# Optimization experiments

Measured on AMD Instinct MI355X. Metric: run time of the kernel, lower is better.

The kernel has to match this reference:

```python
import jax, jax.numpy as jnp
from jax import lax
import numpy as np

T_NO = 50       # history / kernel half-length (hard-coded in module)
T_MAX = 101     # basis kernel length = 2*T_NO + 1
BASIS_NO = 34
HIST_BASIS_NO = 18
SIGMA = 3.0
HID = 20
SUB = 20


def _make_basis(n_basis, length):
    # basis[i, t] = exp(-(t - 3*i)^2 / sigma)
    raw = jnp.arange(length, dtype=jnp.float32)
    pts = 3.0 * jnp.arange(n_basis, dtype=jnp.float32)
    return jnp.exp(-((raw[None, :] - pts[:, None]) ** 2) / SIGMA)


def _conv1d(x, kern, pad):
    # x: [1, Cin, T], kern: [Cout, Cin, K] -> [1, Cout, T'] (torch F.conv1d semantics, cross-correlation)
    return lax.conv_general_dilated(x, kern, window_strides=(1,), padding=[(pad, pad)],
                                    dimension_numbers=('NCH', 'OIH', 'NCH'))


def setup_inputs() -> dict:
    key = jax.random.key(0)
    ks = jax.random.split(key, 12)
    T, Ee, Ei = 200000, 500, 100
    S_e = (jax.random.uniform(ks[0], (T, Ee)) < 0.05).astype(jnp.float32)
    S_i = (jax.random.uniform(ks[1], (T, Ei)) < 0.05).astype(jnp.float32)
    # one-hot synapse->subunit connectivity, as in the original model
    C_syn_e = jax.nn.one_hot(jax.random.randint(ks[2], (Ee,), 0, SUB), SUB, dtype=jnp.float32).T
    C_syn_i = jax.nn.one_hot(jax.random.randint(ks[3], (Ei,), 0, SUB), SUB, dtype=jnp.float32).T
    weight1 = 0.01 * jax.random.normal(ks[4], (HID, 2 * SUB, BASIS_NO), dtype=jnp.float32)
    weight4 = 0.01 * jax.random.normal(ks[5], (1, HID, BASIS_NO), dtype=jnp.float32)
    W_hist = 0.01 * jax.random.normal(ks[6], (HIST_BASIS_NO,), dtype=jnp.float32)
    Theta = 0.01 * jax.random.normal(ks[7], (1,), dtype=jnp.float32)
    W_spk = jnp.ones((1,), jnp.float32)
    Tau_spk = 3.0 * jnp.ones((1,), jnp.float32)
    u = jax.random.uniform(ks[8], (T,), dtype=jnp.float32)  # bernoulli noise
    return dict(S_e=S_e, S_i=S_i, C_syn_e=C_syn_e, C_syn_i=C_syn_i,
                weight1=weight1, weight4=weight4, W_hist=W_hist, Theta=Theta,
                W_spk=W_spk, Tau_spk=Tau_spk, u=u)


def reference(S_e, S_i, C_syn_e, C_syn_i, weight1, weight4, W_hist, Theta, W_spk, Tau_spk, u):
    basis = _make_basis(BASIS_NO, T_MAX)          # [34, 101]
    hist_basis = _make_basis(HIST_BASIS_NO, T_NO)  # [18, 50]

    kern1 = jnp.einsum('hsb,bt->hst', weight1, basis)  # [HID, 2*SUB, 101]
    kern4 = jnp.einsum('ohb,bt->oht', weight4, basis)  # [1, HID, 101]

    # route synapses to subunits, stack e/i: [1, 2*SUB, T]
    syn_in = jnp.concatenate([S_e @ C_syn_e.T, S_i @ C_syn_i.T], axis=1).T[None]
    out1 = jax.nn.leaky_relu(_conv1d(syn_in, kern1, T_NO), 0.01)  # [1, HID, T]
    out4 = _conv1d(out1, kern4, T_NO)[0, 0]                        # [T]

    hist_kern = W_hist @ hist_basis  # [50]
    theta = Theta[0]

    def step(buf, inp):
        # buf: last T_NO spikes, oldest first (== spk_out[t:t+T_NO])
        o_t, u_t = inp
        p = jax.nn.sigmoid(o_t + buf @ hist_kern + theta)
        spk = (u_t < p).astype(jnp.float32)  # torch.bernoulli(p)
        buf = jnp.concatenate([buf[1:], spk[None]])
        return buf, (p, spk)

    buf0 = jnp.zeros((T_NO,), jnp.float32)
    _, (prob_out, spikes) = lax.scan(step, buf0, (out4, u))
    spk_out = jnp.concatenate([jnp.zeros((T_NO,), jnp.float32), spikes])  # [T + T_NO]

    t = jnp.arange(T_NO, dtype=jnp.float32)
    t_tau = t / (Tau_spk[0] ** 2)
    spk_kern = t_tau * jnp.exp(-t_tau) * (W_spk[0] ** 2)  # unflipped; torch flips then cross-correlates
    # torch conv1d(x, flip(k), valid) == jnp.convolve(x, k, 'valid')
    spk_filt = jnp.convolve(spk_out, spk_kern, mode='valid')[:-1]  # [T]
    return (spk_filt, prob_out)
```

## Files before the change

kernel.cpp:

```cpp
#include <hip/hip_runtime.h>
#include <math.h>

#define T_TOT  200000
#define EE     500
#define EI     100
#define SUBN   20
#define NCH    40
#define HIDN   20
#define BNO    34
#define TM     101
#define TNO    50
#define HBNO   18
#define TT1    256
#define EPSF   2e-5f

#define PADL   64
#define PADR   256
#define SROW   (PADL + T_TOT + PADR)

#define GROW   (T_TOT + 112)

#define C1T    1024

#define RTILE  512
#define RHALO  64
#define RRND   3
#define NTILE  ((T_TOT + 1023) / 1024)

__global__ void k_setup(const float* __restrict__ Ce, const float* __restrict__ Ci,
                        const float* __restrict__ Wh, const float* __restrict__ Wspk,
                        const float* __restrict__ Tau,
                        int* __restrict__ ae, int* __restrict__ ai,
                        float* __restrict__ hkpos, float* __restrict__ hkneg,
                        float* __restrict__ spkk, float* __restrict__ gtap,
                        double* __restrict__ hkd, double* __restrict__ basisd)
{
    int tid = threadIdx.x;
    if (tid < EE) {
        int a = 0;
        for (int s = 0; s < SUBN; ++s) if (Ce[s * EE + tid] > 0.5f) a = s;
        ae[tid] = a;
    } else if (tid < EE + EI) {
        int e = tid - EE; int a = 0;
        for (int s = 0; s < SUBN; ++s) if (Ci[s * EI + e] > 0.5f) a = s;
        ai[e] = a;
    } else if (tid < 664) {
        int j = tid - 600;
        double hk = 0.0;
        if (j >= 1 && j <= TNO) {
            int i = TNO - j;
            for (int b = 0; b < HBNO; ++b) {
                double d = (double)i - 3.0 * (double)b;
                hk += (double)Wh[b] * exp(-d * d / 3.0);
            }
        }
        hkd[j] = hk;
        hkpos[j] = (float)fmax(hk, 0.0);
        hkneg[j] = (float)fmin(hk, 0.0);
    } else if (tid < 728) {
        int m = tid - 664; float v = 0.f;
        if (m < TNO) {
            double tau2 = (double)Tau[0] * (double)Tau[0];
            double tt = (double)m / tau2;
            v = (float)(tt * exp(-tt) * (double)Wspk[0] * (double)Wspk[0]);
        }
        spkk[m] = v;
    } else if (tid < 753) {
        int j = tid - 740;
        gtap[tid - 728] = (float)exp(-(double)(j * j) / 3.0);
    }
    for (int idx = tid; idx < BNO * TM; idx += blockDim.x) {
        int b = idx / TM, k = idx % TM;
        double d = (double)k - 3.0 * (double)b;
        basisd[idx] = exp(-d * d / 3.0);
    }
}

__global__ void k_prep(const float* __restrict__ w1, const float* __restrict__ w4,
                       const double* __restrict__ basisd,
                       float* __restrict__ kern4, float* __restrict__ w1T,
                       float* __restrict__ dtab, float* __restrict__ syn)
{
    int idx = blockIdx.x * 256 + threadIdx.x;
    if (idx < HIDN * TM) {
        int h = idx % HIDN, k = idx / HIDN;
        double acc = 0.0;
        for (int b = 0; b < BNO; ++b) acc += (double)w4[h * BNO + b] * basisd[b * TM + k];
        kern4[k * HIDN + h] = (float)acc;
    } else if (idx < 2020 + NCH * BNO * HIDN) {
        int j = idx - 2020;
        int h = j % HIDN, b = (j / HIDN) % BNO, s = j / (HIDN * BNO);
        w1T[j] = w1[(h * NCH + s) * BNO + b];
    } else if (idx < 29220 + NCH * 24 * HIDN) {
        int j = idx - 29220;
        int h = j % HIDN, mi = (j / HIDN) % 24, s = j / (HIDN * 24);
        int m = (mi < 12) ? (mi - 62) : (mi + 39);
        double acc = 0.0;
        for (int b = 0; b < BNO; ++b) {
            int jj = m + 50 - 3 * b;
            if (jj >= -12 && jj <= 12)
                acc += (double)w1[(h * NCH + s) * BNO + b] * exp(-(double)(jj * jj) / 3.0);
        }
        dtab[j] = (float)acc;
    } else if (idx < 48420 + NCH * (PADL + PADR)) {
        int j = idx - 48420;
        int r = j / (PADL + PADR), c = j % (PADL + PADR);
        int off = (c < PADL) ? c : (PADL + T_TOT + (c - PADL));
        syn[(size_t)r * SROW + off] = 0.f;
    }
}

__global__ __launch_bounds__(256) void k_route(const float* __restrict__ Se,
                                               const float* __restrict__ Si,
                                               const int* __restrict__ ae,
                                               const int* __restrict__ ai,
                                               float* __restrict__ syn)
{
    __shared__ float acc[NCH * 64];
    __shared__ int sae[EE];
    __shared__ int sai[EI];
    int tid = threadIdx.x;
    for (int i = tid; i < NCH * 64; i += 256) acc[i] = 0.f;
    for (int i = tid; i < EE; i += 256) sae[i] = ae[i];
    for (int i = tid; i < EI; i += 256) sai[i] = ai[i];
    __syncthreads();
    int t0 = blockIdx.x * 64;
    int lane = tid & 63, grp = tid >> 6;
    for (int ec = 0; ec < 8; ++ec) {
        int e = ec * 64 + lane;
        if (e < EE) {
            int a = sae[e];
            for (int ts = grp; ts < 64; ts += 4) {
                float v = Se[(size_t)(t0 + ts) * EE + e];
                if (v != 0.f) atomicAdd(&acc[a * 64 + ts], v);
            }
        }
    }
    for (int ec = 0; ec < 2; ++ec) {
        int e = ec * 64 + lane;
        if (e < EI) {
            int a = sai[e] + SUBN;
            for (int ts = grp; ts < 64; ts += 4) {
                float v = Si[(size_t)(t0 + ts) * EI + e];
                if (v != 0.f) atomicAdd(&acc[a * 64 + ts], v);
            }
        }
    }
    __syncthreads();
    for (int i = tid; i < NCH * 64; i += 256) {
        int s = i >> 6, ts = i & 63;
        syn[(size_t)s * SROW + PADL + t0 + ts] = acc[i];
    }
}

__global__ __launch_bounds__(256) void k_prefilt(const float* __restrict__ syn,
                                                 const float* __restrict__ gtap,
                                                 float* __restrict__ G)
{
    int gi = blockIdx.x * 256 + threadIdx.x;
    if (gi >= GROW) return;
    const float* sp = syn + (size_t)blockIdx.y * SROW + PADL + (gi - 50);
    double a = 0.0;
#pragma unroll
    for (int j = -12; j <= 12; ++j)
        a += (double)gtap[j + 12] * (double)sp[j];
    G[(size_t)blockIdx.y * GROW + gi] = (float)a;
}

__global__ __launch_bounds__(256) void k_conv1f(const float* __restrict__ G,
                                                const float* __restrict__ syn,
                                                const float* __restrict__ w1T,
                                                const float* __restrict__ dtab,
                                                float* __restrict__ out1)
{
    int part = blockIdx.x & 3;
    int tile = blockIdx.x >> 2;
    int h0 = part * 5;
    int t = tile * C1T + 4 * threadIdx.x;
    if (t >= T_TOT) return;
    float acc[5][4];
#pragma unroll
    for (int hh = 0; hh < 5; ++hh)
#pragma unroll
        for (int tt = 0; tt < 4; ++tt) acc[hh][tt] = 0.f;

    for (int s = 0; s < NCH; ++s) {
        const float* wp = w1T + (s * BNO) * HIDN + h0;
        const float* Gp = G + (size_t)s * GROW + t;
        const float* dp = dtab + (s * 24) * HIDN + h0;
        const float* sp = syn + (size_t)s * SROW + PADL + t;
#pragma unroll 2
        for (int b = 0; b < BNO; ++b) {
            float c[5], gv[4];
#pragma unroll
            for (int hh = 0; hh < 5; ++hh) c[hh] = wp[b * HIDN + hh];
#pragma unroll
            for (int tt = 0; tt < 4; ++tt) gv[tt] = Gp[3 * b + tt];
#pragma unroll
            for (int hh = 0; hh < 5; ++hh)
#pragma unroll
                for (int tt = 0; tt < 4; ++tt)
                    acc[hh][tt] = fmaf(c[hh], gv[tt], acc[hh][tt]);
        }
#pragma unroll
        for (int mi = 0; mi < 24; ++mi) {
            int mo = (mi < 12) ? (mi - 62) : (mi + 39);
            float c[5], xv[4];
#pragma unroll
            for (int hh = 0; hh < 5; ++hh) c[hh] = dp[mi * HIDN + hh];
#pragma unroll
            for (int tt = 0; tt < 4; ++tt) xv[tt] = sp[mo + tt];
#pragma unroll
            for (int hh = 0; hh < 5; ++hh)
#pragma unroll
                for (int tt = 0; tt < 4; ++tt)
                    acc[hh][tt] = fmaf(-c[hh], xv[tt], acc[hh][tt]);
        }
    }
#pragma unroll
    for (int hh = 0; hh < 5; ++hh) {
        float4 st;
        float o0 = acc[hh][0], o1 = acc[hh][1], o2 = acc[hh][2], o3 = acc[hh][3];
        st.x = (o0 > 0.f) ? o0 : 0.01f * o0;
        st.y = (o1 > 0.f) ? o1 : 0.01f * o1;
        st.z = (o2 > 0.f) ? o2 : 0.01f * o2;
        st.w = (o3 > 0.f) ? o3 : 0.01f * o3;
        *(float4*)(out1 + (size_t)(h0 + hh) * T_TOT + t) = st;
    }
}

__global__ __launch_bounds__(256) void k_conv2(const float* __restrict__ out1,
                                               const float* __restrict__ kern4,
                                               const float* __restrict__ Theta,
                                               const float* __restrict__ u,
                                               double* __restrict__ xd,
                                               double* __restrict__ thrd,
                                               float* __restrict__ thr32)
{
    __shared__ float s1[HIDN * (TT1 + 100)];
    int tid = threadIdx.x;
    int t0 = blockIdx.x * TT1;
    for (int i = tid; i < HIDN * (TT1 + 100); i += 256) {
        int h = i / (TT1 + 100), x = i % (TT1 + 100);
        int g = t0 + x - TNO;
        s1[i] = (g >= 0 && g < T_TOT) ? out1[(size_t)h * T_TOT + g] : 0.f;
    }
    __syncthreads();
    int t = t0 + tid;
    if (t >= T_TOT) return;
    double acc = 0.0;
    for (int k = 0; k < TM; ++k) {
        const float* kp = kern4 + k * HIDN;
#pragma unroll
        for (int h = 0; h < HIDN; ++h)
            acc = fma((double)s1[h * (TT1 + 100) + tid + k], (double)kp[h], acc);
    }
    double x = acc + (double)Theta[0];
    double uu = (double)u[t];
    double th = (log(uu) - log1p(-uu)) - x;
    xd[t] = x; thrd[t] = th; thr32[t] = (float)th;
}

__global__ void k_init(float* __restrict__ blo, float* __restrict__ bhi,
                       int* __restrict__ dirty)
{
    int i = blockIdx.x * 256 + threadIdx.x;
    if (i < T_TOT + 64) {
        blo[i] = 0.f;
        bhi[i] = (i >= TNO && i < T_TOT + TNO) ? 1.f : 0.f;
    }
    if (i < 256) dirty[i] = 0;
}

__global__ __launch_bounds__(256) void k_relax(const float* __restrict__ thr32,
                                               const float* __restrict__ hkpos,
                                               const float* __restrict__ hkneg,
                                               float* __restrict__ blo,
                                               float* __restrict__ bhi)
{
    __shared__ float slo[RTILE + RHALO], shi[RTILE + RHALO];
    __shared__ float sth[RTILE + RHALO];
    __shared__ float shp[64], shn[64];
    int tid = threadIdx.x;
    int t0 = blockIdx.x * RTILE;
    for (int i = tid; i < RTILE + RHALO; i += 256) {
        int t = t0 - RHALO + i;
        int g = t + TNO;
        bool ok = (g >= 0 && g < T_TOT + 64);
        slo[i] = ok ? blo[g] : 0.f;
        shi[i] = ok ? bhi[g] : 0.f;
        sth[i] = (t >= 0 && t < T_TOT) ? thr32[t] : 0.f;
    }
    if (tid < 64) { shp[tid] = hkpos[tid]; shn[tid] = hkneg[tid]; }
    __syncthreads();
    for (int r = 0; r < RRND; ++r) {
        for (int i = tid; i < RTILE + RHALO; i += 256) {
            if (i < TNO) continue;
            float l = slo[i], h = shi[i];
            if (l == h) continue;
            float lo = 0.f, hi = 0.f;
            for (int j = 1; j <= TNO; ++j) {
                float bl = slo[i - j], bh = shi[i - j];
                float hp = shp[j], hn = shn[j];
                lo = fmaf(hp, bl, lo); lo = fmaf(hn, bh, lo);
                hi = fmaf(hp, bh, hi); hi = fmaf(hn, bl, hi);
            }
            float th = sth[i];
            if (lo > th + EPSF)      slo[i] = 1.f;
            else if (hi < th - EPSF) shi[i] = 0.f;
        }
        __syncthreads();
    }
    for (int i = tid; i < RTILE; i += 256) {
        int t = t0 + i;
        if (t < T_TOT) {
            blo[t + TNO] = slo[RHALO + i];
            bhi[t + TNO] = shi[RHALO + i];
        }
    }
}

__global__ __launch_bounds__(1024) void k_mark(const float* __restrict__ blo,
                                               const float* __restrict__ bhi,
                                               int* __restrict__ dirty)
{
    int t = blockIdx.x * 1024 + threadIdx.x;
    int unk = (t < T_TOT) && (blo[t + TNO] != bhi[t + TNO]);
    int c = __syncthreads_count(unk);
    if (threadIdx.x == 0) dirty[blockIdx.x] = c;
}

__global__ __launch_bounds__(1024) void k_compact(const float* __restrict__ blo,
                                                  const float* __restrict__ bhi,
                                                  const int* __restrict__ dirty,
                                                  int* __restrict__ list,
                                                  int* __restrict__ utot)
{
    __shared__ int wsum[16];
    __shared__ int sbase;
    int tid = threadIdx.x;
    int t = blockIdx.x * 1024 + tid;
    int unk = (t < T_TOT) && (blo[t + TNO] != bhi[t + TNO]);
    unsigned long long m = __ballot(unk);
    int lane = tid & 63, wv = tid >> 6;
    int lr = __popcll(m & ((1ull << lane) - 1ull));
    if (lane == 0) wsum[wv] = __popcll(m);
    if (tid == 0) {
        int b = 0;
        for (int k = 0; k < (int)blockIdx.x; ++k) b += dirty[k];
        sbase = b;
        if (blockIdx.x == 0) {
            int tot = 0;
            for (int k = 0; k < NTILE; ++k) tot += dirty[k];
            utot[0] = tot;
        }
    }
    __syncthreads();
    if (tid == 0) {
        int r = 0;
        for (int k = 0; k < 16; ++k) { int c = wsum[k]; wsum[k] = r; r += c; }
    }
    __syncthreads();
    if (unk) list[sbase + wsum[wv] + lr] = t;
}

__global__ __launch_bounds__(256) void k_afix(const int* __restrict__ list,
                                              const int* __restrict__ utot,
                                              const float* __restrict__ blo,
                                              const double* __restrict__ hkd,
                                              double* __restrict__ afix)
{
    int i = blockIdx.x * 256 + threadIdx.x;
    if (i >= utot[0]) return;
    int t = list[i];
    double a = 0.0;
    for (int j = 1; j <= TNO; ++j)
        a += hkd[j] * (double)blo[t - j + TNO];
    afix[i] = a;
}

__global__ __launch_bounds__(64) void k_resolve(const int* __restrict__ list,
                                                const double* __restrict__ afix,
                                                const double* __restrict__ thrd,
                                                const double* __restrict__ hkd,
                                                const int* __restrict__ utot,
                                                float* __restrict__ blo,
                                                float* __restrict__ bhi)
{
    __shared__ int    lt[128];
    __shared__ double la[128];
    __shared__ double lth[128];
    __shared__ int    lb[128];
    __shared__ double shk[64];
    int lane = threadIdx.x;
    shk[lane] = (lane >= 1 && lane <= TNO) ? hkd[lane] : 0.0;
    int U = utot[0];
    for (int i0 = 0; i0 < U; i0 += 64) {
        int i = i0 + lane;
        if (i < U) {
            int t = list[i];
            lt[i & 127] = t;
            la[i & 127] = afix[i];
            lth[i & 127] = thrd[t];
        }
        __syncthreads();
        if (lane == 0) {
            int n = (U - i0 < 64) ? (U - i0) : 64;
            for (int q = 0; q < n; ++q) {
                int ii = i0 + q, c = ii & 127;
                int t = lt[c];
                double a = la[c];
                for (int k = ii - 1; k >= 0; --k) {
                    int ck = k & 127;
                    int tk = lt[ck];
                    if (tk < t - TNO) break;
                    if (lb[ck]) a += shk[t - tk];
                }
                int sbit = (a > lth[c]) ? 1 : 0;
                lb[c] = sbit;
                float f = (float)sbit;
                blo[t + TNO] = f; bhi[t + TNO] = f;
            }
        }
        __syncthreads();
    }
}

__global__ __launch_bounds__(256) void k_out(const float* __restrict__ blo,
                                             const float* __restrict__ spkk,
                                             const double* __restrict__ hkd,
                                             const double* __restrict__ xd,
                                             float* __restrict__ outp)
{
    __shared__ float sb[TT1 + 64];
    __shared__ float ssp[64];
    __shared__ double shk[64];
    int tid = threadIdx.x;
    int t0 = blockIdx.x * TT1;
    for (int i = tid; i < TT1 + TNO; i += 256) {
        int g = t0 + i;
        sb[i] = (g < T_TOT + 64) ? blo[g] : 0.f;
    }
    if (tid < 64) { ssp[tid] = spkk[tid]; shk[tid] = hkd[tid]; }
    __syncthreads();
    int t = t0 + tid;
    if (t >= T_TOT) return;
    float filt = 0.f;
    double a = 0.0;
    for (int m = 1; m <= TNO; ++m) {
        float b = sb[tid + TNO - m];
        filt = fmaf(b, ssp[m - 1], filt);
        a += shk[m] * (double)b;
    }
    double p = 1.0 / (1.0 + exp(-(xd[t] + a)));
    outp[t] = filt;
    outp[T_TOT + t] = (float)p;
}

extern "C" void kernel_launch(void* const* d_in, const int* in_sizes, int n_in,
                              void* d_out, int out_size, void* d_ws, size_t ws_size,
                              hipStream_t stream)
{
    (void)in_sizes; (void)n_in; (void)out_size; (void)ws_size;
    const float* Se = (const float*)d_in[0];
    const float* Si = (const float*)d_in[1];
    const float* Ce = (const float*)d_in[2];
    const float* Ci = (const float*)d_in[3];
    const float* w1 = (const float*)d_in[4];
    const float* w4 = (const float*)d_in[5];
    const float* Wh = (const float*)d_in[6];
    const float* Th = (const float*)d_in[7];
    const float* Ws = (const float*)d_in[8];
    const float* Ta = (const float*)d_in[9];
    const float* u  = (const float*)d_in[10];

    char* w = (char*)d_ws;
    size_t off = 0;
    auto alloc = [&](size_t n) { size_t o = off; off += (n + 15) & ~(size_t)15; return o; };

    size_t gzone = alloc((size_t)NCH * GROW * 4);
    float*  G     = (float*)(w + gzone);
    {
        char* z = w + gzone; size_t zo = 0;
        auto za = [&](size_t n) { size_t o = zo; zo += (n + 15) & ~(size_t)15; return o; };
        (void)za;
    }
    double* xd    = (double*)(w + gzone);
    double* thrd  = (double*)(w + gzone + 1600000);
    float*  thr32 = (float*)(w + gzone + 3200000);
    float*  blo   = (float*)(w + gzone + 4000000);
    float*  bhi   = (float*)(w + gzone + 4801024);
    int*    dirty = (int*)(w + gzone + 5602048);
    int*    list  = (int*)(w + gzone + 5604096);
    double* afix  = (double*)(w + gzone + 6404096);
    int*    utot  = dirty + 200;

    float*  syn    = (float*)(w + alloc((size_t)NCH * SROW * 4));
    float*  out1   = (float*)(w + alloc((size_t)HIDN * T_TOT * 4));
    float*  kern4  = (float*)(w + alloc((size_t)TM * HIDN * 4));
    float*  w1T    = (float*)(w + alloc((size_t)NCH * BNO * HIDN * 4));
    float*  dtab   = (float*)(w + alloc((size_t)NCH * 24 * HIDN * 4));
    double* basisd = (double*)(w + alloc((size_t)BNO * TM * 8));
    int*    ae     = (int*)(w + alloc(EE * 4));
    int*    ai     = (int*)(w + alloc(EI * 4));
    float*  hkpos  = (float*)(w + alloc(64 * 4));
    float*  hkneg  = (float*)(w + alloc(64 * 4));
    float*  spkk   = (float*)(w + alloc(64 * 4));
    float*  gtap   = (float*)(w + alloc(32 * 4));
    double* hkd    = (double*)(w + alloc(64 * 8));

    k_setup<<<1, 1024, 0, stream>>>(Ce, Ci, Wh, Ws, Ta, ae, ai, hkpos, hkneg, spkk, gtap, hkd, basisd);
    k_prep<<<(48420 + NCH * (PADL + PADR) + 255) / 256, 256, 0, stream>>>(w1, w4, basisd, kern4, w1T, dtab, syn);
    k_route<<<T_TOT / 64, 256, 0, stream>>>(Se, Si, ae, ai, syn);
    dim3 pg((GROW + 255) / 256, NCH);
    k_prefilt<<<pg, 256, 0, stream>>>(syn, gtap, G);
    k_conv1f<<<((T_TOT + C1T - 1) / C1T) * 4, 256, 0, stream>>>(G, syn, w1T, dtab, out1);
    k_conv2<<<(T_TOT + TT1 - 1) / TT1, 256, 0, stream>>>(out1, kern4, Th, u, xd, thrd, thr32);
    k_init<<<(T_TOT + 64 + 255) / 256, 256, 0, stream>>>(blo, bhi, dirty);
    for (int r = 0; r < 4; ++r)
        k_relax<<<(T_TOT + RTILE - 1) / RTILE, 256, 0, stream>>>(thr32, hkpos, hkneg, blo, bhi);
    k_mark<<<NTILE, 1024, 0, stream>>>(blo, bhi, dirty);
    k_compact<<<NTILE, 1024, 0, stream>>>(blo, bhi, dirty, list, utot);
    k_afix<<<(T_TOT + 255) / 256, 256, 0, stream>>>(list, utot, blo, hkd, afix);
    k_resolve<<<1, 64, 0, stream>>>(list, afix, thrd, hkd, utot, blo, bhi);
    k_out<<<(T_TOT + TT1 - 1) / TT1, 256, 0, stream>>>(blo, spkk, hkd, xd, (float*)d_out);
}
```

Baseline: 1.229 ms.

## Parallelize unresolved spike chains, vectorize routing, and retile conv1 per timestep

```diff
diff --git a/kernel.cpp b/kernel.cpp
--- a/kernel.cpp
+++ b/kernel.cpp
@@ -19,8 +19,6 @@
 #define SROW   (PADL + T_TOT + PADR)
 
 #define GROW   (T_TOT + 112)
-
-#define C1T    1024
 
 #define RTILE  512
 #define RHALO  64
@@ -126,23 +124,31 @@
     __syncthreads();
     int t0 = blockIdx.x * 64;
     int lane = tid & 63, grp = tid >> 6;
-    for (int ec = 0; ec < 8; ++ec) {
-        int e = ec * 64 + lane;
-        if (e < EE) {
-            int a = sae[e];
+    for (int ec = 0; ec < 2; ++ec) {
+        int ev = ec * 64 + lane;
+        if (ev < EE / 4) {
+            int e = 4 * ev;
+            int a0 = sae[e], a1 = sae[e + 1], a2 = sae[e + 2], a3 = sae[e + 3];
             for (int ts = grp; ts < 64; ts += 4) {
-                float v = Se[(size_t)(t0 + ts) * EE + e];
-                if (v != 0.f) atomicAdd(&acc[a * 64 + ts], v);
+                float4 v = *(const float4*)(Se + (size_t)(t0 + ts) * EE + e);
+                if (v.x != 0.f) atomicAdd(&acc[a0 * 64 + ts], v.x);
+                if (v.y != 0.f) atomicAdd(&acc[a1 * 64 + ts], v.y);
+                if (v.z != 0.f) atomicAdd(&acc[a2 * 64 + ts], v.z);
+                if (v.w != 0.f) atomicAdd(&acc[a3 * 64 + ts], v.w);
             }
         }
     }
-    for (int ec = 0; ec < 2; ++ec) {
-        int e = ec * 64 + lane;
-        if (e < EI) {
-            int a = sai[e] + SUBN;
+    {
+        int ev = lane;
+        if (ev < EI / 4) {
+            int e = 4 * ev;
+            int a0 = sai[e] + SUBN, a1 = sai[e + 1] + SUBN, a2 = sai[e + 2] + SUBN, a3 = sai[e + 3] + SUBN;
             for (int ts = grp; ts < 64; ts += 4) {
-                float v = Si[(size_t)(t0 + ts) * EI + e];
-                if (v != 0.f) atomicAdd(&acc[a * 64 + ts], v);
+                float4 v = *(const float4*)(Si + (size_t)(t0 + ts) * EI + e);
+                if (v.x != 0.f) atomicAdd(&acc[a0 * 64 + ts], v.x);
+                if (v.y != 0.f) atomicAdd(&acc[a1 * 64 + ts], v.y);
+                if (v.z != 0.f) atomicAdd(&acc[a2 * 64 + ts], v.z);
+                if (v.w != 0.f) atomicAdd(&acc[a3 * 64 + ts], v.w);
             }
         }
     }
@@ -167,65 +173,49 @@
     G[(size_t)blockIdx.y * GROW + gi] = (float)a;
 }
 
-__global__ __launch_bounds__(256) void k_conv1f(const float* __restrict__ G,
-                                                const float* __restrict__ syn,
-                                                const float* __restrict__ w1T,
-                                                const float* __restrict__ dtab,
-                                                float* __restrict__ out1)
-{
-    int part = blockIdx.x & 3;
-    int tile = blockIdx.x >> 2;
-    int h0 = part * 5;
-    int t = tile * C1T + 4 * threadIdx.x;
+__global__ __launch_bounds__(256, 3) void k_conv1f(const float* __restrict__ G,
+                                                   const float* __restrict__ syn,
+                                                   const float* __restrict__ w1T,
+                                                   const float* __restrict__ dtab,
+                                                   float* __restrict__ out1)
+{
+    int t = blockIdx.x * 256 + threadIdx.x;
     if (t >= T_TOT) return;
-    float acc[5][4];
-#pragma unroll
-    for (int hh = 0; hh < 5; ++hh)
-#pragma unroll
-        for (int tt = 0; tt < 4; ++tt) acc[hh][tt] = 0.f;
+    float acc[HIDN];
+#pragma unroll
+    for (int h = 0; h < HIDN; ++h) acc[h] = 0.f;
 
     for (int s = 0; s < NCH; ++s) {
-        const float* wp = w1T + (s * BNO) * HIDN + h0;
+        const float* wp = w1T + (s * BNO) * HIDN;
         const float* Gp = G + (size_t)s * GROW + t;
-        const float* dp = dtab + (s * 24) * HIDN + h0;
+        const float* dp = dtab + (s * 24) * HIDN;
         const float* sp = syn + (size_t)s * SROW + PADL + t;
 #pragma unroll 2
         for (int b = 0; b < BNO; ++b) {
-            float c[5], gv[4];
-#pragma unroll
-            for (int hh = 0; hh < 5; ++hh) c[hh] = wp[b * HIDN + hh];
-#pragma unroll
-            for (int tt = 0; tt < 4; ++tt) gv[tt] = Gp[3 * b + tt];
-#pragma unroll
-            for (int hh = 0; hh < 5; ++hh)
-#pragma unroll
-                for (int tt = 0; tt < 4; ++tt)
-                    acc[hh][tt] = fmaf(c[hh], gv[tt], acc[hh][tt]);
-        }
-#pragma unroll
-        for (int mi = 0; mi < 24; ++mi) {
-            int mo = (mi < 12) ? (mi - 62) : (mi + 39);
-            float c[5], xv[4];
-#pragma unroll
-            for (int hh = 0; hh < 5; ++hh) c[hh] = dp[mi * HIDN + hh];
-#pragma unroll
-            for (int tt = 0; tt < 4; ++tt) xv[tt] = sp[mo + tt];
-#pragma unroll
-            for (int hh = 0; hh < 5; ++hh)
-#pragma unroll
-                for (int tt = 0; tt < 4; ++tt)
-                    acc[hh][tt] = fmaf(-c[hh], xv[tt], acc[hh][tt]);
-        }
-    }
-#pragma unroll
-    for (int hh = 0; hh < 5; ++hh) {
-        float4 st;
-        float o0 = acc[hh][0], o1 = acc[hh][1], o2 = acc[hh][2], o3 = acc[hh][3];
-        st.x = (o0 > 0.f) ? o0 : 0.01f * o0;
-        st.y = (o1 > 0.f) ? o1 : 0.01f * o1;
-        st.z = (o2 > 0.f) ? o2 : 0.01f * o2;
-        st.w = (o3 > 0.f) ? o3 : 0.01f * o3;
-        *(float4*)(out1 + (size_t)(h0 + hh) * T_TOT + t) = st;
+            float gv = Gp[3 * b];
+#pragma unroll
+            for (int h = 0; h < HIDN; ++h)
+                acc[h] = fmaf(wp[b * HIDN + h], gv, acc[h]);
+        }
+#pragma unroll 2
+        for (int mi = 0; mi < 12; ++mi) {
+            float xv = sp[mi - 62];
+#pragma unroll
+            for (int h = 0; h < HIDN; ++h)
+                acc[h] = fmaf(-dp[mi * HIDN + h], xv, acc[h]);
+        }
+#pragma unroll 2
+        for (int mi = 12; mi < 24; ++mi) {
+            float xv = sp[mi + 39];
+#pragma unroll
+            for (int h = 0; h < HIDN; ++h)
+                acc[h] = fmaf(-dp[mi * HIDN + h], xv, acc[h]);
+        }
+    }
+#pragma unroll
+    for (int h = 0; h < HIDN; ++h) {
+        float o = acc[h];
+        out1[(size_t)h * T_TOT + t] = (o > 0.f) ? o : 0.01f * o;
     }
 }
 
@@ -337,26 +327,26 @@
                                                   int* __restrict__ utot)
 {
     __shared__ int wsum[16];
+    __shared__ int sd[NTILE];
     __shared__ int sbase;
     int tid = threadIdx.x;
+    if (tid < NTILE) sd[tid] = dirty[tid];
     int t = blockIdx.x * 1024 + tid;
     int unk = (t < T_TOT) && (blo[t + TNO] != bhi[t + TNO]);
     unsigned long long m = __ballot(unk);
     int lane = tid & 63, wv = tid >> 6;
     int lr = __popcll(m & ((1ull << lane) - 1ull));
     if (lane == 0) wsum[wv] = __popcll(m);
+    __syncthreads();
     if (tid == 0) {
         int b = 0;
-        for (int k = 0; k < (int)blockIdx.x; ++k) b += dirty[k];
+        for (int k = 0; k < (int)blockIdx.x; ++k) b += sd[k];
         sbase = b;
         if (blockIdx.x == 0) {
             int tot = 0;
-            for (int k = 0; k < NTILE; ++k) tot += dirty[k];
+            for (int k = 0; k < NTILE; ++k) tot += sd[k];
             utot[0] = tot;
         }
-    }
-    __syncthreads();
-    if (tid == 0) {
         int r = 0;
         for (int k = 0; k < 16; ++k) { int c = wsum[k]; wsum[k] = r; r += c; }
     }
@@ -379,50 +369,67 @@
     afix[i] = a;
 }
 
-__global__ __launch_bounds__(64) void k_resolve(const int* __restrict__ list,
-                                                const double* __restrict__ afix,
-                                                const double* __restrict__ thrd,
-                                                const double* __restrict__ hkd,
-                                                const int* __restrict__ utot,
-                                                float* __restrict__ blo,
-                                                float* __restrict__ bhi)
-{
-    __shared__ int    lt[128];
-    __shared__ double la[128];
-    __shared__ double lth[128];
-    __shared__ int    lb[128];
+__global__ __launch_bounds__(256) void k_chain(const int* __restrict__ list,
+                                               int* __restrict__ utot,
+                                               int* __restrict__ chead)
+{
+    __shared__ int wcnt[4];
+    __shared__ int base_s;
+    int tid = threadIdx.x, lane = tid & 63, wv = tid >> 6;
+    int U = utot[0];
+    if (tid == 0) base_s = 0;
+    __syncthreads();
+    for (int b0 = 0; b0 < U; b0 += 256) {
+        int i = b0 + tid;
+        int head = 0;
+        if (i < U) head = (i == 0) || (list[i] - list[i - 1] > TNO);
+        unsigned long long m = __ballot(head);
+        int pre = __popcll(m & ((1ull << lane) - 1ull));
+        if (lane == 0) wcnt[wv] = __popcll(m);
+        __syncthreads();
+        int wbase = 0;
+        for (int k = 0; k < wv; ++k) wbase += wcnt[k];
+        int tot = wcnt[0] + wcnt[1] + wcnt[2] + wcnt[3];
+        if (head) chead[base_s + wbase + pre] = i;
+        __syncthreads();
+        if (tid == 0) base_s += tot;
+        __syncthreads();
+    }
+    if (tid == 0) utot[1] = base_s;
+}
+
+__global__ __launch_bounds__(256) void k_cresolve(const int* __restrict__ list,
+                                                  const int* __restrict__ chead,
+                                                  const double* __restrict__ afix,
+                                                  const double* __restrict__ thrd,
+                                                  const double* __restrict__ hkd,
+                                                  const int* __restrict__ utot,
+                                                  int* bits,
+                                                  float* __restrict__ blo,
+                                                  float* __restrict__ bhi)
+{
     __shared__ double shk[64];
-    int lane = threadIdx.x;
-    shk[lane] = (lane >= 1 && lane <= TNO) ? hkd[lane] : 0.0;
-    int U = utot[0];
-    for (int i0 = 0; i0 < U; i0 += 64) {
-        int i = i0 + lane;
-        if (i < U) {
-            int t = list[i];
-            lt[i & 127] = t;
-            la[i & 127] = afix[i];
-            lth[i & 127] = thrd[t];
-        }
-        __syncthreads();
-        if (lane == 0) {
-            int n = (U - i0 < 64) ? (U - i0) : 64;
-            for (int q = 0; q < n; ++q) {
-                int ii = i0 + q, c = ii & 127;
-                int t = lt[c];
-                double a = la[c];
-                for (int k = ii - 1; k >= 0; --k) {
-                    int ck = k & 127;
-                    int tk = lt[ck];
-                    if (tk < t - TNO) break;
-                    if (lb[ck]) a += shk[t - tk];
-                }
-                int sbit = (a > lth[c]) ? 1 : 0;
-                lb[c] = sbit;
-                float f = (float)sbit;
-                blo[t + TNO] = f; bhi[t + TNO] = f;
-            }
-        }
-        __syncthreads();
+    if (threadIdx.x < 64)
+        shk[threadIdx.x] = (threadIdx.x >= 1 && threadIdx.x <= TNO) ? hkd[threadIdx.x] : 0.0;
+    __syncthreads();
+    int c = blockIdx.x * 256 + threadIdx.x;
+    int nch = utot[1];
+    if (c >= nch) return;
+    int i0 = chead[c];
+    int i1 = (c + 1 < nch) ? chead[c + 1] : utot[0];
+    for (int i = i0; i < i1; ++i) {
+        int t = list[i];
+        double a = afix[i];
+        for (int k = i - 1; k >= i0; --k) {
+            int dt = t - list[k];
+            if (dt > TNO) break;
+            if (bits[k]) a += shk[dt];
+        }
+        int sb = (a > thrd[t]) ? 1 : 0;
+        bits[i] = sb;
+        float f = (float)sb;
+        blo[t + TNO] = f;
+        bhi[t + TNO] = f;
     }
 }
 
@@ -480,19 +487,16 @@
 
     size_t gzone = alloc((size_t)NCH * GROW * 4);
     float*  G     = (float*)(w + gzone);
-    {
-        char* z = w + gzone; size_t zo = 0;
-        auto za = [&](size_t n) { size_t o = zo; zo += (n + 15) & ~(size_t)15; return o; };
-        (void)za;
-    }
     double* xd    = (double*)(w + gzone);
     double* thrd  = (double*)(w + gzone + 1600000);
     float*  thr32 = (float*)(w + gzone + 3200000);
     float*  blo   = (float*)(w + gzone + 4000000);
-    float*  bhi   = (float*)(w + gzone + 4801024);
-    int*    dirty = (int*)(w + gzone + 5602048);
-    int*    list  = (int*)(w + gzone + 5604096);
-    double* afix  = (double*)(w + gzone + 6404096);
+    float*  bhi   = (float*)(w + gzone + 4800512);
+    int*    dirty = (int*)(w + gzone + 5600768);
+    int*    list  = (int*)(w + gzone + 5601792);
+    double* afix  = (double*)(w + gzone + 6401792);
+    int*    chead = (int*)(w + gzone + 8001792);
+    int*    bits  = (int*)(w + gzone + 8801800);
     int*    utot  = dirty + 200;
 
     float*  syn    = (float*)(w + alloc((size_t)NCH * SROW * 4));
@@ -514,14 +518,15 @@
     k_route<<<T_TOT / 64, 256, 0, stream>>>(Se, Si, ae, ai, syn);
     dim3 pg((GROW + 255) / 256, NCH);
     k_prefilt<<<pg, 256, 0, stream>>>(syn, gtap, G);
-    k_conv1f<<<((T_TOT + C1T - 1) / C1T) * 4, 256, 0, stream>>>(G, syn, w1T, dtab, out1);
+    k_conv1f<<<(T_TOT + 255) / 256, 256, 0, stream>>>(G, syn, w1T, dtab, out1);
     k_conv2<<<(T_TOT + TT1 - 1) / TT1, 256, 0, stream>>>(out1, kern4, Th, u, xd, thrd, thr32);
     k_init<<<(T_TOT + 64 + 255) / 256, 256, 0, stream>>>(blo, bhi, dirty);
     for (int r = 0; r < 4; ++r)
         k_relax<<<(T_TOT + RTILE - 1) / RTILE, 256, 0, stream>>>(thr32, hkpos, hkneg, blo, bhi);
     k_mark<<<NTILE, 1024, 0, stream>>>(blo, bhi, dirty);
     k_compact<<<NTILE, 1024, 0, stream>>>(blo, bhi, dirty, list, utot);
+    k_chain<<<1, 256, 0, stream>>>(list, utot, chead);
     k_afix<<<(T_TOT + 255) / 256, 256, 0, stream>>>(list, utot, blo, hkd, afix);
-    k_resolve<<<1, 64, 0, stream>>>(list, afix, thrd, hkd, utot, blo, bhi);
+    k_cresolve<<<(T_TOT + 255) / 256, 256, 0, stream>>>(list, chead, afix, thrd, hkd, utot, bits, blo, bhi);
     k_out<<<(T_TOT + TT1 - 1) / TT1, 256, 0, stream>>>(blo, spkk, hkd, xd, (float*)d_out);
 }
```

New measurement: 1.187 ms. -3.4%, faster.
